# Performance work log

Hardware: AMD Instinct MI355X
Metric: run time of the kernel (lower is better)

The kernel has to match this reference:

```python
import jax, jax.numpy as jnp
import numpy as np

NUM_TERMS = 8
NUM_CHANNELS = 64
BATCH = 8
NODES = 2048


def setup_inputs() -> dict:
    key = jax.random.key(0)
    kA, kh = jax.random.split(key)
    A = jax.random.normal(kA, (BATCH, NODES, NODES), dtype=jnp.float32)
    # xavier_uniform over (num_terms+1, num_channels)
    fan_in, fan_out = NUM_TERMS + 1, NUM_CHANNELS
    limit = float(np.sqrt(6.0 / (fan_in + fan_out)))
    h = jax.random.uniform(kh, (NUM_TERMS + 1, NUM_CHANNELS), dtype=jnp.float32,
                           minval=-limit, maxval=limit)
    return {"A": A, "h": h}


def reference(A, h):
    # Y[b,n,c] = h[0,c] + sum_{i=1..T} h[i,c] * diag(A^i)[b,n]
    num_terms = h.shape[0] - 1
    diags = []  # each [B, N]: diagonal of A^i
    Ap = A
    for i in range(num_terms):
        if i > 0:
            Ap = jnp.matmul(Ap, A)  # A^(i+1), computed once per power
        diags.append(jnp.diagonal(Ap, axis1=-2, axis2=-1))
    D = jnp.stack(diags, axis=0)  # [T, B, N]
    # fuse per-channel weighted sum of diagonals into one einsum
    out = jnp.einsum("tbn,tc->bnc", D, h[1:])
    out = out + h[0][None, None, :]  # identity term: diag(I) == 1
    return out
```

## Files before the change

kernel.cpp:

```cpp
#include <hip/hip_runtime.h>
#include <hip/hip_bf16.h>

#define NN 2048
#define BB 8
#define NC 64
#define NTILE 32
#define NITER 16

typedef __bf16 bf16_8 __attribute__((ext_vector_type(8)));
typedef __bf16 bf16_4 __attribute__((ext_vector_type(4)));
typedef float f32x16 __attribute__((ext_vector_type(16)));

__device__ __forceinline__ void gll16(const void* g, void* l) {
  __builtin_amdgcn_global_load_lds((const __attribute__((address_space(1))) void*)g,
                                   (__attribute__((address_space(3))) void*)l,
                                   16, 0, 0);
}

__global__ __launch_bounds__(256)
void k_convert(const float* __restrict__ A, __bf16* __restrict__ Ab, __bf16* __restrict__ At) {
  __shared__ __bf16 tile[64][65];
  int b = blockIdx.z;
  const float* Asrc = A + (size_t)b * NN * NN;
  __bf16* Abd = Ab + (size_t)b * NN * NN;
  __bf16* Atd = At + (size_t)b * NN * NN;
  int r0 = blockIdx.y * 64, c0 = blockIdx.x * 64;
  int row = threadIdx.x >> 4;
  int col4 = (threadIdx.x & 15) * 4;
#pragma unroll
  for (int rr = 0; rr < 64; rr += 16) {
    float4 v = *(const float4*)&Asrc[(size_t)(r0 + row + rr) * NN + c0 + col4];
    bf16_4 hv;
    hv[0] = (__bf16)v.x; hv[1] = (__bf16)v.y; hv[2] = (__bf16)v.z; hv[3] = (__bf16)v.w;
    *(bf16_4*)&Abd[(size_t)(r0 + row + rr) * NN + c0 + col4] = hv;
    tile[row + rr][col4 + 0] = hv[0];
    tile[row + rr][col4 + 1] = hv[1];
    tile[row + rr][col4 + 2] = hv[2];
    tile[row + rr][col4 + 3] = hv[3];
  }
  __syncthreads();
  int row2 = threadIdx.x >> 3;
  int col8 = (threadIdx.x & 7) * 8;
#pragma unroll
  for (int rr = 0; rr < 64; rr += 32) {
    bf16_8 v;
#pragma unroll
    for (int j = 0; j < 8; ++j) v[j] = tile[col8 + j][row2 + rr];
    *(bf16_8*)&Atd[(size_t)(c0 + row2 + rr) * NN + r0 + col8] = v;
  }
}

__device__ __forceinline__
void gemm_body256(const __bf16* __restrict__ Pb, const __bf16* __restrict__ Qb,
                  __bf16* __restrict__ Cb, __bf16* __restrict__ Ctb,
                  __bf16* smem, int tmBlk, int tnBlk) {
  __bf16 (*As)[256][64] = (__bf16(*)[256][64])smem;
  __bf16 (*Bs)[256][64] = (__bf16(*)[256][64])(smem + 32768);
  const int tid = threadIdx.x;
  const int wave = tid >> 6, lane = tid & 63;
  const int wm = wave >> 2, wn = wave & 3;
  const int tm = tmBlk * 256, tn = tnBlk * 256;
  const int am = lane & 31, ah = lane >> 5, rx = am & 7;

  const int sr = lane >> 3;
  const int sc = (lane & 7) ^ sr;
  const __bf16* srcA = Pb + (size_t)(tm + wave * 8 + sr) * NN + sc * 8;
  const __bf16* srcB = Qb + (size_t)(tn + wave * 8 + sr) * NN + sc * 8;

#define STAGE(Tc_, s_, bufT_)                                                  \
  do {                                                                         \
    if ((s_) == 0) {                                                 \
      const __bf16* s0 = srcA + (size_t)(Tc_) * 64;                            \
      gll16(s0,                   &As[bufT_][wave * 8][0]);                    \
      gll16(s0 + (size_t)64 * NN, &As[bufT_][64 + wave * 8][0]);               \
    } else if ((s_) == 1) {                                          \
      const __bf16* s0 = srcB + (size_t)128 * NN + (size_t)(Tc_) * 64;         \
      gll16(s0,                   &Bs[bufT_][128 + wave * 8][0]);              \
      gll16(s0 + (size_t)64 * NN, &Bs[bufT_][192 + wave * 8][0]);              \
    } else if ((s_) == 2) {                                          \
      const __bf16* s0 = srcA + (size_t)128 * NN + (size_t)(Tc_) * 64;         \
      gll16(s0,                   &As[bufT_][128 + wave * 8][0]);              \
      gll16(s0 + (size_t)64 * NN, &As[bufT_][192 + wave * 8][0]);              \
    } else {                                                         \
      const __bf16* s0 = srcB + (size_t)(Tc_) * 64;                            \
      gll16(s0,                   &Bs[bufT_][wave * 8][0]);                    \
      gll16(s0 + (size_t)64 * NN, &Bs[bufT_][64 + wave * 8][0]);               \
    }                                                                          \
  } while (0)

  STAGE(0, 0, 0); STAGE(0, 3, 0); STAGE(0, 2, 0); STAGE(0, 1, 0);
  STAGE(1, 0, 1); STAGE(1, 2, 1); STAGE(1, 1, 1);
  asm volatile("s_waitcnt vmcnt(6)" ::: "memory");
  __builtin_amdgcn_s_barrier();

  f32x16 acc[4][2] = {};
  bf16_8 af[2][4];

  for (int it = 0; it < NITER; ++it) {
#pragma unroll
    for (int p = 0; p < 8; ++p) {
      const int q = p & 3;
      const int rbuf = p >> 2;
      const int i0 = (q >> 1) * 2;
      const int in = (q == 1 || q == 2) ? 1 : 0;
      if ((q & 1) == 0) {
#pragma unroll
        for (int i = 0; i < 2; ++i) {
          const int ra = (2 * (i0 + i) + wm) * 32 + am;
#pragma unroll
          for (int ks = 0; ks < 4; ++ks)
            af[i][ks] = *(const bf16_8*)&As[rbuf][ra][((2 * ks + ah) ^ rx) * 8];
        }
      }
      bf16_8 bfr[4];
      {
        const int rb = (in * 4 + wn) * 32 + am;
#pragma unroll
        for (int ks = 0; ks < 4; ++ks)
          bfr[ks] = *(const bf16_8*)&Bs[rbuf][rb][((2 * ks + ah) ^ rx) * 8];
      }
      if (p == 0) {
        int T = 2 * it + 1; STAGE(T, 3, 1);
      } else if (p == 1) {
        int T = 2 * it + 2; if (T > NTILE - 1) T = NTILE - 1;
        STAGE(T, 0, 0);
      } else if (p == 3) {
        int T = 2 * it + 2; if (T > NTILE - 1) T = NTILE - 1;
        STAGE(T, 2, 0); STAGE(T, 1, 0);
      } else if (p == 4) {
        int T = 2 * it + 2; if (T > NTILE - 1) T = NTILE - 1;
        STAGE(T, 3, 0);
      } else if (p == 5) {
        int T = 2 * it + 3; if (T > NTILE - 1) T = NTILE - 1;
        STAGE(T, 0, 1);
      } else if (p == 7) {
        int T = 2 * it + 3; if (T > NTILE - 1) T = NTILE - 1;
        STAGE(T, 2, 1); STAGE(T, 1, 1);
      }
      __builtin_amdgcn_s_barrier();
      asm volatile("s_waitcnt lgkmcnt(0)" ::: "memory");
      __builtin_amdgcn_s_setprio(1);
#pragma unroll
      for (int ks = 0; ks < 4; ++ks)
#pragma unroll
        for (int i = 0; i < 2; ++i)
          acc[i0 + i][in] = __builtin_amdgcn_mfma_f32_32x32x16_bf16(
              af[i][ks], bfr[ks], acc[i0 + i][in], 0, 0, 0);
      __builtin_amdgcn_s_setprio(0);
      if (q == 3) asm volatile("s_waitcnt vmcnt(6)" ::: "memory");
      __builtin_amdgcn_s_barrier();
    }
  }
  asm volatile("s_waitcnt vmcnt(0)" ::: "memory");

  const int cc = am;
  const int rq = ah * 4;
#pragma unroll
  for (int im = 0; im < 4; ++im)
#pragma unroll
    for (int in = 0; in < 2; ++in)
#pragma unroll
      for (int reg = 0; reg < 16; ++reg) {
        int row = (reg & 3) + 8 * (reg >> 2) + rq;
        Cb[(size_t)(tm + (2 * im + wm) * 32 + row) * NN +
           (tn + (4 * in + wn) * 32 + cc)] = (__bf16)acc[im][in][reg];
      }

  if (Ctb != nullptr) {
    __syncthreads();
    __bf16 (*Tt)[264] = (__bf16(*)[264])smem;
#pragma unroll
    for (int ch = 0; ch < 4; ++ch) {
      if ((wn >> 1) == (ch & 1)) {
        const int inw = ch >> 1;
#pragma unroll
        for (int im = 0; im < 4; ++im)
#pragma unroll
          for (int g = 0; g < 4; ++g) {
            bf16_4 v;
#pragma unroll
            for (int r = 0; r < 4; ++r) v[r] = (__bf16)acc[im][inw][g * 4 + r];
            *(bf16_4*)&Tt[(wn & 1) * 32 + cc][(2 * im + wm) * 32 + 8 * g + rq] = v;
          }
      }
      __syncthreads();
#pragma unroll
      for (int rr = 0; rr < 4; ++rr) {
        int trow = rr * 16 + (tid >> 5);
        int tcol = (tid & 31) * 8;
        bf16_8 v = *(const bf16_8*)&Tt[trow][tcol];
        *(bf16_8*)&Ctb[(size_t)(tn + ch * 64 + trow) * NN + tm + tcol] = v;
      }
      __syncthreads();
    }
  }
#undef STAGE
}

__global__ __launch_bounds__(512, 2)
void k_gemm1(const __bf16* __restrict__ Ab, const __bf16* __restrict__ At,
             __bf16* __restrict__ A2, __bf16* __restrict__ A2t) {
  __shared__ __align__(16) __bf16 smem[65536];
  size_t mb = (size_t)blockIdx.z * NN * NN;
  gemm_body256(Ab + mb, At + mb, A2 + mb, A2t + mb, smem, blockIdx.y, blockIdx.x);
}

__global__ __launch_bounds__(512, 2)
void k_gemm23(const __bf16* __restrict__ At, const __bf16* __restrict__ A2,
              const __bf16* __restrict__ A2t,
              __bf16* __restrict__ A3t, __bf16* __restrict__ A4,
              __bf16* __restrict__ A4t) {
  __shared__ __align__(16) __bf16 smem[65536];
  int job = blockIdx.z >> 3;
  size_t mb = (size_t)(blockIdx.z & 7) * NN * NN;
  if (job == 0)
    gemm_body256(At + mb, A2 + mb, A3t + mb, nullptr, smem, blockIdx.y, blockIdx.x);
  else
    gemm_body256(A2 + mb, A2t + mb, A4 + mb, A4t + mb, smem, blockIdx.y, blockIdx.x);
}

__global__ __launch_bounds__(256)
void k_reduce(const float* __restrict__ A, const float* __restrict__ h,
              const __bf16* __restrict__ A2, const __bf16* __restrict__ A3t,
              const __bf16* __restrict__ A4, const __bf16* __restrict__ A4t,
              float* __restrict__ out) {
  int b = blockIdx.y;
  int wave = threadIdx.x >> 6, lane = threadIdx.x & 63;
  int n = blockIdx.x * 4 + wave;
  size_t mb = (size_t)b * NN * NN;
  size_t rb = mb + (size_t)n * NN;
  float d5 = 0, d6 = 0, d7 = 0, d8 = 0;
  for (int c = 0; c < NN; c += 512) {
    int k = c + lane * 8;
    bf16_8 va2  = *(const bf16_8*)(A2 + rb + k);
    bf16_8 va3t = *(const bf16_8*)(A3t + rb + k);
    bf16_8 va4  = *(const bf16_8*)(A4 + rb + k);
    bf16_8 va4t = *(const bf16_8*)(A4t + rb + k);
#pragma unroll
    for (int j = 0; j < 8; ++j) {
      float f2 = (float)va2[j], f4 = (float)va4[j];
      float f3t = (float)va3t[j], f4t = (float)va4t[j];
      d5 += f2 * f3t;
      d6 += f2 * f4t;
      d7 += f4 * f3t;
      d8 += f4 * f4t;
    }
  }
#pragma unroll
  for (int off = 32; off > 0; off >>= 1) {
    d5 += __shfl_xor(d5, off);
    d6 += __shfl_xor(d6, off);
    d7 += __shfl_xor(d7, off);
    d8 += __shfl_xor(d8, off);
  }
  float d1 = A[mb + (size_t)n * NN + n];
  float d2 = (float)A2[rb + n];
  float d3 = (float)A3t[rb + n];
  float d4 = (float)A4[rb + n];
  float r = h[lane] + h[64 + lane] * d1 + h[128 + lane] * d2 + h[192 + lane] * d3 +
            h[256 + lane] * d4 + h[320 + lane] * d5 + h[384 + lane] * d6 +
            h[448 + lane] * d7 + h[512 + lane] * d8;
  out[((size_t)b * NN + n) * NC + lane] = r;
}

extern "C" void kernel_launch(void* const* d_in, const int* in_sizes, int n_in,
                              void* d_out, int out_size, void* d_ws, size_t ws_size,
                              hipStream_t stream) {
  const float* A = (const float*)d_in[0];
  const float* h = (const float*)d_in[1];
  float* out = (float*)d_out;

  size_t elems = (size_t)BB * NN * NN;
  __bf16* Ab  = (__bf16*)d_ws;
  __bf16* At  = Ab + elems;
  __bf16* A2  = At + elems;
  __bf16* A2t = A2 + elems;
  __bf16* A3t = A2t + elems;
  __bf16* A4  = A3t + elems;
  __bf16* A4t = Ab;

  k_convert<<<dim3(32, 32, BB), dim3(256), 0, stream>>>(A, Ab, At);
  k_gemm1<<<dim3(8, 8, BB), dim3(512), 0, stream>>>(Ab, At, A2, A2t);
  k_gemm23<<<dim3(8, 8, 2 * BB), dim3(512), 0, stream>>>(At, A2, A2t, A3t, A4, A4t);
  k_reduce<<<dim3(NN / 4, BB), dim3(256), 0, stream>>>(A, h, A2, A3t, A4, A4t, out);
}
```

Before: 696.9 us.

## Keep B fragments in registers and prefetch next tile's B during MFMA phase

```diff
diff --git a/kernel.cpp b/kernel.cpp
--- a/kernel.cpp
+++ b/kernel.cpp
@@ -89,12 +89,19 @@
   } while (0)
 
   STAGE(0, 0, 0); STAGE(0, 3, 0); STAGE(0, 2, 0); STAGE(0, 1, 0);
-  STAGE(1, 0, 1); STAGE(1, 2, 1); STAGE(1, 1, 1);
-  asm volatile("s_waitcnt vmcnt(6)" ::: "memory");
+  STAGE(1, 0, 1); STAGE(1, 3, 1); STAGE(1, 2, 1); STAGE(1, 1, 1);
+  asm volatile("s_waitcnt vmcnt(8)" ::: "memory");
   __builtin_amdgcn_s_barrier();
 
   f32x16 acc[4][2] = {};
-  bf16_8 af[2][4];
+  bf16_8 af[2][4], bfr[2][4];
+
+  {
+    const int rb0 = wn * 32 + am;
+#pragma unroll
+    for (int ks = 0; ks < 4; ++ks)
+      bfr[0][ks] = *(const bf16_8*)&Bs[0][rb0][((2 * ks + ah) ^ rx) * 8];
+  }
 
   for (int it = 0; it < NITER; ++it) {
 #pragma unroll
@@ -103,55 +110,69 @@
       const int rbuf = p >> 2;
       const int i0 = (q >> 1) * 2;
       const int in = (q == 1 || q == 2) ? 1 : 0;
-      if ((q & 1) == 0) {
+      if (q == 0) {
 #pragma unroll
         for (int i = 0; i < 2; ++i) {
-          const int ra = (2 * (i0 + i) + wm) * 32 + am;
+          const int ra = (2 * i + wm) * 32 + am;
 #pragma unroll
           for (int ks = 0; ks < 4; ++ks)
             af[i][ks] = *(const bf16_8*)&As[rbuf][ra][((2 * ks + ah) ^ rx) * 8];
         }
-      }
-      bf16_8 bfr[4];
-      {
-        const int rb = (in * 4 + wn) * 32 + am;
+      } else if (q == 1) {
+        const int rb1 = (4 + wn) * 32 + am;
 #pragma unroll
         for (int ks = 0; ks < 4; ++ks)
-          bfr[ks] = *(const bf16_8*)&Bs[rbuf][rb][((2 * ks + ah) ^ rx) * 8];
-      }
-      if (p == 0) {
-        int T = 2 * it + 1; STAGE(T, 3, 1);
-      } else if (p == 1) {
+          bfr[1][ks] = *(const bf16_8*)&Bs[rbuf][rb1][((2 * ks + ah) ^ rx) * 8];
+      } else if (q == 2) {
+#pragma unroll
+        for (int i = 0; i < 2; ++i) {
+          const int ra = (4 + 2 * i + wm) * 32 + am;
+#pragma unroll
+          for (int ks = 0; ks < 4; ++ks)
+            af[i][ks] = *(const bf16_8*)&As[rbuf][ra][((2 * ks + ah) ^ rx) * 8];
+        }
+      }
+      if (p == 1) {
         int T = 2 * it + 2; if (T > NTILE - 1) T = NTILE - 1;
-        STAGE(T, 0, 0);
+        STAGE(T, 0, 0); STAGE(T, 3, 0);
+      } else if (p == 2) {
+        int T = 2 * it + 2; if (T > NTILE - 1) T = NTILE - 1;
+        STAGE(T, 1, 0);
       } else if (p == 3) {
         int T = 2 * it + 2; if (T > NTILE - 1) T = NTILE - 1;
-        STAGE(T, 2, 0); STAGE(T, 1, 0);
-      } else if (p == 4) {
-        int T = 2 * it + 2; if (T > NTILE - 1) T = NTILE - 1;
-        STAGE(T, 3, 0);
+        STAGE(T, 2, 0);
       } else if (p == 5) {
         int T = 2 * it + 3; if (T > NTILE - 1) T = NTILE - 1;
-        STAGE(T, 0, 1);
+        STAGE(T, 0, 1); STAGE(T, 3, 1);
+      } else if (p == 6) {
+        int T = 2 * it + 3; if (T > NTILE - 1) T = NTILE - 1;
+        STAGE(T, 1, 1);
       } else if (p == 7) {
         int T = 2 * it + 3; if (T > NTILE - 1) T = NTILE - 1;
-        STAGE(T, 2, 1); STAGE(T, 1, 1);
-      }
+        STAGE(T, 2, 1);
+      }
+
+      if (q == 3) asm volatile("s_waitcnt vmcnt(8)" ::: "memory");
       __builtin_amdgcn_s_barrier();
-      asm volatile("s_waitcnt lgkmcnt(0)" ::: "memory");
+      if (q != 3) asm volatile("s_waitcnt lgkmcnt(0)" ::: "memory");
       __builtin_amdgcn_s_setprio(1);
 #pragma unroll
       for (int ks = 0; ks < 4; ++ks)
 #pragma unroll
         for (int i = 0; i < 2; ++i)
           acc[i0 + i][in] = __builtin_amdgcn_mfma_f32_32x32x16_bf16(
-              af[i][ks], bfr[ks], acc[i0 + i][in], 0, 0, 0);
+              af[i][ks], bfr[in][ks], acc[i0 + i][in], 0, 0, 0);
       __builtin_amdgcn_s_setprio(0);
-      if (q == 3) asm volatile("s_waitcnt vmcnt(6)" ::: "memory");
+      if (q == 3) {
+        const int rb0 = wn * 32 + am;
+#pragma unroll
+        for (int ks = 0; ks < 4; ++ks)
+          bfr[0][ks] = *(const bf16_8*)&Bs[rbuf ^ 1][rb0][((2 * ks + ah) ^ rx) * 8];
+      }
       __builtin_amdgcn_s_barrier();
     }
   }
-  asm volatile("s_waitcnt vmcnt(0)" ::: "memory");
+  asm volatile("s_waitcnt vmcnt(0) lgkmcnt(0)" ::: "memory");
 
   const int cc = am;
   const int rq = ah * 4;
```

Result: faster. 652.8 us (-6.3%).
